# Kernel tuning notes

Hardware: AMD Instinct MI355X
Metric: run time of the kernel (lower is better)

The kernel has to match this reference:

```python
import jax, jax.numpy as jnp
import numpy as np

N_NODES = 50000
N_EDGES = 800000


def _glorot(key, shape):
    fan_in, fan_out = shape
    lim = float(np.sqrt(6.0 / (fan_in + fan_out)))
    return jax.random.uniform(key, shape, jnp.float32, -lim, lim)


def setup_inputs() -> dict:
    key = jax.random.key(0)
    ks = jax.random.split(key, 8)
    x = jax.random.normal(ks[0], (N_NODES, 2), jnp.float32)
    edge_index = jax.random.randint(ks[1], (2, N_EDGES), 0, N_NODES, jnp.int64)
    edge_weight = jax.random.uniform(ks[2], (N_EDGES,), jnp.float32)
    return {
        "x": x,
        "edge_index": edge_index,
        "edge_weight": edge_weight,
        "W1": _glorot(ks[3], (2, 128)),
        "b1": jnp.zeros((128,), jnp.float32),
        "W2": _glorot(ks[4], (128, 64)),
        "b2": jnp.zeros((64,), jnp.float32),
        "W3": _glorot(ks[5], (64, 1)),
        "b3": jnp.zeros((1,), jnp.float32),
    }


def _gcn_conv(x, W, b, src, dst, ew, n_nodes):
    # PyG GCNConv with normalize=False: out[i] = sum_{e:(j->i)} ew[e] * (x_j @ W) + b
    h = x @ W                       # [N, F_out] tiny GEMM
    msg = h[src] * ew[:, None]      # [E, F_out] gather + scale
    out = jax.ops.segment_sum(msg, dst, num_segments=n_nodes)  # scatter-add
    return out + b


def reference(x, edge_index, edge_weight, W1, b1, W2, b2, W3, b3):
    src, dst = edge_index[0], edge_index[1]  # source_to_target flow: aggregate at dst
    n = x.shape[0]
    h1 = jax.nn.relu(_gcn_conv(x, W1, b1, src, dst, edge_weight, n))
    # dropout is a no-op in eval mode
    h2 = jax.nn.relu(_gcn_conv(h1, W2, b2, src, dst, edge_weight, n))
    h3 = _gcn_conv(h2, W3, b3, src, dst, edge_weight, n)  # [N, 1]
    return h3.squeeze(-1)  # [N]
```

## Files before the change

### kernel.cpp

```cpp
#include <hip/hip_runtime.h>
#include <hip/hip_fp16.h>

#define N_NODES 50000
#define N_EDGES 800000
#define BSHIFT 8
#define NBKT ((N_NODES + 255) >> BSHIFT)
#define CAP 8192
#define P1_EDGES 4096
#define P1_BLOCKS ((N_EDGES + P1_EDGES - 1) / P1_EDGES)
#define BIN_THREADS 1024
#define SORT_THREADS 512
#define SORT_LDS_CAP 6144

__global__ void bin_edges(const int* __restrict__ src, const int* __restrict__ dst,
                          const float* __restrict__ ew, int* __restrict__ bcur,
                          unsigned* __restrict__ bpk, unsigned char* __restrict__ bdl) {
    __shared__ unsigned spk[P1_EDGES];
    __shared__ unsigned short sdst[P1_EDGES];
    __shared__ int cnt[NBKT];
    __shared__ int cbase[NBKT];
    int t = threadIdx.x;
    if (t < NBKT) cnt[t] = 0;
    __syncthreads();
    int e0 = blockIdx.x * P1_EDGES;
    for (int k = 0; k < P1_EDGES / BIN_THREADS; k++) {
        int i = k * BIN_THREADS + t;
        int e = e0 + i;
        if (e < N_EDGES) {
            int d = dst[e];
            unsigned hw = (unsigned)__half_as_ushort(__float2half(ew[e]));
            spk[i] = (unsigned)src[e] | (hw << 16);
            sdst[i] = (unsigned short)d;
            atomicAdd(&cnt[d >> BSHIFT], 1);
        }
    }
    __syncthreads();
    if (t < NBKT) {
        int v = cnt[t];
        int base = v ? atomicAdd(&bcur[t], v) : 0;
        cbase[t] = t * CAP + base;
        cnt[t] = 0;
    }
    __syncthreads();
    int nmax = N_EDGES - e0;
    if (nmax > P1_EDGES) nmax = P1_EDGES;
    for (int k = 0; k < P1_EDGES / BIN_THREADS; k++) {
        int i = k * BIN_THREADS + t;
        if (i < nmax) {
            int d = sdst[i];
            int b = d >> BSHIFT;
            int pos = cbase[b] + atomicAdd(&cnt[b], 1);
            bpk[pos] = spk[i];
            bdl[pos] = (unsigned char)(d & 255);
        }
    }
}

__global__ void sort_bucket(const int* __restrict__ bcur, const unsigned* __restrict__ bpk,
                            const unsigned char* __restrict__ bdl,
                            unsigned* __restrict__ sorted, int2* __restrict__ rowspan) {
    __shared__ unsigned spk[SORT_LDS_CAP];
    __shared__ unsigned char sdl[SORT_LDS_CAP];
    __shared__ int nh[256];
    __shared__ int scn[256];
    __shared__ int lcur[256];
    int b = blockIdx.x;
    int t = threadIdx.x;
    int base = b * CAP;
    int n = bcur[b];
    if (n > CAP) n = CAP;
    bool lds_path = (n <= SORT_LDS_CAP);
    if (t < 256) nh[t] = 0;
    __syncthreads();
    if (lds_path) {
        for (int e = t; e < n; e += SORT_THREADS) {
            spk[e] = bpk[base + e];
            unsigned char d = bdl[base + e];
            sdl[e] = d;
            atomicAdd(&nh[d], 1);
        }
    } else {
        for (int e = t; e < n; e += SORT_THREADS)
            atomicAdd(&nh[bdl[base + e]], 1);
    }
    __syncthreads();
    int v = 0;
    if (t < 256) { v = nh[t]; scn[t] = v; }
    __syncthreads();
    for (int off = 1; off < 256; off <<= 1) {
        int u = (t < 256 && t >= off) ? scn[t - off] : 0;
        __syncthreads();
        if (t < 256) scn[t] += u;
        __syncthreads();
    }
    if (t < 256) {
        int ex = scn[t] - v;
        int node = (b << BSHIFT) + t;
        if (node < N_NODES) rowspan[node] = make_int2(base + ex, base + ex + v);
        nh[t] = ex;
        lcur[t] = 0;
    }
    __syncthreads();
    if (lds_path) {
        for (int e = t; e < n; e += SORT_THREADS) {
            int dlow = sdl[e];
            int pos = base + nh[dlow] + atomicAdd(&lcur[dlow], 1);
            sorted[pos] = spk[e];
        }
    } else {
        for (int e = t; e < n; e += SORT_THREADS) {
            int dlow = bdl[base + e];
            int pos = base + nh[dlow] + atomicAdd(&lcur[dlow], 1);
            sorted[pos] = bpk[base + e];
        }
    }
}

__device__ __forceinline__ float edge_w(unsigned p) {
    return __half2float(__ushort_as_half((unsigned short)(p >> 16)));
}

#define L1_NODES_PER_BLOCK 32
__global__ void fused_l1(const int2* __restrict__ rowspan, const unsigned* __restrict__ sorted,
                         const float* __restrict__ x, const float* __restrict__ W1,
                         const float* __restrict__ b1, const float* __restrict__ W2,
                         __half* __restrict__ t2) {
    __shared__ float w2s[128 * 64];
    __shared__ float hls[4][8][128];
    for (int k = threadIdx.x; k < 128 * 64; k += 256) w2s[k] = W2[k];
    int wave = threadIdx.x >> 6;
    int lane = threadIdx.x & 63;
    float w1a = W1[lane],      w1b = W1[128 + lane];
    float w1c = W1[64 + lane], w1d = W1[192 + lane];
    float b1lo = b1[lane], b1hi = b1[64 + lane];
    __syncthreads();

    int sub = lane >> 4;
    int sl  = lane & 15;
    int base = blockIdx.x * L1_NODES_PER_BLOCK + wave * 8;

#pragma unroll
    for (int g = 0; g < 2; g++) {
        int gnode = base + g * 4 + sub;
        float a0 = 0.f, a1 = 0.f;
        if (gnode < N_NODES) {
            int2 sp = rowspan[gnode];
            for (int e = sp.x + sl; e < sp.y; e += 16) {
                unsigned p = sorted[e];
                float w = edge_w(p);
                float2 xv = ((const float2*)x)[p & 0xFFFF];
                a0 = fmaf(w, xv.x, a0);
                a1 = fmaf(w, xv.y, a1);
            }
        }
#pragma unroll
        for (int off = 1; off < 16; off <<= 1) {
            a0 += __shfl_xor(a0, off);
            a1 += __shfl_xor(a1, off);
        }
#pragma unroll
        for (int n = 0; n < 4; n++) {
            float an0 = __shfl(a0, 16 * n);
            float an1 = __shfl(a1, 16 * n);
            float hlo = fmaxf(fmaf(an0, w1a, fmaf(an1, w1b, b1lo)), 0.f);
            float hhi = fmaxf(fmaf(an0, w1c, fmaf(an1, w1d, b1hi)), 0.f);
            hls[wave][g * 4 + n][lane] = hlo;
            hls[wave][g * 4 + n][64 + lane] = hhi;
        }
    }
    float acc[8] = {0.f, 0.f, 0.f, 0.f, 0.f, 0.f, 0.f, 0.f};
#pragma unroll 2
    for (int k4 = 0; k4 < 32; k4++) {
        float w0 = w2s[(4 * k4 + 0) * 64 + lane];
        float w1 = w2s[(4 * k4 + 1) * 64 + lane];
        float w2 = w2s[(4 * k4 + 2) * 64 + lane];
        float w3 = w2s[(4 * k4 + 3) * 64 + lane];
#pragma unroll
        for (int n = 0; n < 8; n++) {
            float4 h = *(const float4*)&hls[wave][n][4 * k4];
            acc[n] = fmaf(h.x, w0, fmaf(h.y, w1, fmaf(h.z, w2, fmaf(h.w, w3, acc[n]))));
        }
    }
#pragma unroll
    for (int n = 0; n < 8; n++)
        if (base + n < N_NODES) t2[(base + n) * 64 + lane] = __float2half(acc[n]);
}

__global__ void gather2_dot3(const int2* __restrict__ rowspan, const unsigned* __restrict__ sorted,
                             const __half* __restrict__ t2, const float* __restrict__ b2,
                             const float* __restrict__ W3, float* __restrict__ t3) {
    int gtid = blockIdx.x * blockDim.x + threadIdx.x;
    int node = gtid >> 6;
    int lane = threadIdx.x & 63;
    if (node >= N_NODES) return;
    int eg  = lane >> 3;
    int fli = lane & 7;
    int2 sp = rowspan[node];
    float a0 = 0.f, a1 = 0.f, a2 = 0.f, a3 = 0.f, a4 = 0.f, a5 = 0.f, a6 = 0.f, a7 = 0.f;
    int e = sp.x + eg;
    for (; e + 8 < sp.y; e += 16) {
        unsigned p0 = sorted[e];
        unsigned p1 = sorted[e + 8];
        uint4 q0 = *(const uint4*)(t2 + (p0 & 0xFFFF) * 64 + fli * 8);
        uint4 q1 = *(const uint4*)(t2 + (p1 & 0xFFFF) * 64 + fli * 8);
        float w0 = edge_w(p0), w1 = edge_w(p1);
        float2 f;
        f = __half22float2(*(const __half2*)&q0.x); a0 = fmaf(w0, f.x, a0); a1 = fmaf(w0, f.y, a1);
        f = __half22float2(*(const __half2*)&q0.y); a2 = fmaf(w0, f.x, a2); a3 = fmaf(w0, f.y, a3);
        f = __half22float2(*(const __half2*)&q0.z); a4 = fmaf(w0, f.x, a4); a5 = fmaf(w0, f.y, a5);
        f = __half22float2(*(const __half2*)&q0.w); a6 = fmaf(w0, f.x, a6); a7 = fmaf(w0, f.y, a7);
        f = __half22float2(*(const __half2*)&q1.x); a0 = fmaf(w1, f.x, a0); a1 = fmaf(w1, f.y, a1);
        f = __half22float2(*(const __half2*)&q1.y); a2 = fmaf(w1, f.x, a2); a3 = fmaf(w1, f.y, a3);
        f = __half22float2(*(const __half2*)&q1.z); a4 = fmaf(w1, f.x, a4); a5 = fmaf(w1, f.y, a5);
        f = __half22float2(*(const __half2*)&q1.w); a6 = fmaf(w1, f.x, a6); a7 = fmaf(w1, f.y, a7);
    }
    if (e < sp.y) {
        unsigned p = sorted[e];
        uint4 q = *(const uint4*)(t2 + (p & 0xFFFF) * 64 + fli * 8);
        float w = edge_w(p);
        float2 f;
        f = __half22float2(*(const __half2*)&q.x); a0 = fmaf(w, f.x, a0); a1 = fmaf(w, f.y, a1);
        f = __half22float2(*(const __half2*)&q.y); a2 = fmaf(w, f.x, a2); a3 = fmaf(w, f.y, a3);
        f = __half22float2(*(const __half2*)&q.z); a4 = fmaf(w, f.x, a4); a5 = fmaf(w, f.y, a5);
        f = __half22float2(*(const __half2*)&q.w); a6 = fmaf(w, f.x, a6); a7 = fmaf(w, f.y, a7);
    }
#pragma unroll
    for (int off = 8; off < 64; off <<= 1) {
        a0 += __shfl_xor(a0, off); a1 += __shfl_xor(a1, off);
        a2 += __shfl_xor(a2, off); a3 += __shfl_xor(a3, off);
        a4 += __shfl_xor(a4, off); a5 += __shfl_xor(a5, off);
        a6 += __shfl_xor(a6, off); a7 += __shfl_xor(a7, off);
    }
    float4 bA = *(const float4*)(b2 + fli * 8);
    float4 bB = *(const float4*)(b2 + fli * 8 + 4);
    float4 wA = *(const float4*)(W3 + fli * 8);
    float4 wB = *(const float4*)(W3 + fli * 8 + 4);
    float h = fmaxf(a0 + bA.x, 0.f) * wA.x + fmaxf(a1 + bA.y, 0.f) * wA.y +
              fmaxf(a2 + bA.z, 0.f) * wA.z + fmaxf(a3 + bA.w, 0.f) * wA.w +
              fmaxf(a4 + bB.x, 0.f) * wB.x + fmaxf(a5 + bB.y, 0.f) * wB.y +
              fmaxf(a6 + bB.z, 0.f) * wB.z + fmaxf(a7 + bB.w, 0.f) * wB.w;
#pragma unroll
    for (int off = 1; off < 8; off <<= 1) h += __shfl_xor(h, off);
    if (lane == 0) t3[node] = h;
}

__global__ void gather3(const int2* __restrict__ rowspan, const unsigned* __restrict__ sorted,
                        const float* __restrict__ t3, const float* __restrict__ b3,
                        float* __restrict__ out) {
    int gtid = blockIdx.x * blockDim.x + threadIdx.x;
    int wid = gtid >> 6;
    int lane = threadIdx.x & 63;
    int sub = lane >> 4;
    int sl  = lane & 15;
    int node = wid * 4 + sub;
    if (node >= N_NODES) return;
    int2 sp = rowspan[node];
    float acc = 0.f;
    for (int e = sp.x + sl; e < sp.y; e += 16) {
        unsigned p = sorted[e];
        acc = fmaf(edge_w(p), t3[p & 0xFFFF], acc);
    }
#pragma unroll
    for (int off = 1; off < 16; off <<= 1) acc += __shfl_xor(acc, off);
    if (sl == 0) out[node] = acc + b3[0];
}

extern "C" void kernel_launch(void* const* d_in, const int* in_sizes, int n_in,
                              void* d_out, int out_size, void* d_ws, size_t ws_size,
                              hipStream_t stream) {
    const float* x  = (const float*)d_in[0];
    const int*   ei = (const int*)d_in[1];
    const float* ew = (const float*)d_in[2];
    const float* W1 = (const float*)d_in[3];
    const float* b1 = (const float*)d_in[4];
    const float* W2 = (const float*)d_in[5];
    const float* b2 = (const float*)d_in[6];
    const float* W3 = (const float*)d_in[7];
    const float* b3 = (const float*)d_in[8];
    float* out = (float*)d_out;

    const int* src = ei;
    const int* dst = ei + N_EDGES;

    char* p = (char*)d_ws;
    int*  bcur    = (int*)p;            p += NBKT * sizeof(int);
    p = (char*)(((uintptr_t)p + 15) & ~(uintptr_t)15);
    int2* rowspan = (int2*)p;           p += N_NODES * sizeof(int2);
    unsigned* bpk = (unsigned*)p;       p += (long)NBKT * CAP * sizeof(unsigned);
    unsigned char* bdl = (unsigned char*)p; p += (long)NBKT * CAP;
    p = (char*)(((uintptr_t)p + 15) & ~(uintptr_t)15);
    unsigned* sorted  = (unsigned*)p;   p += (long)NBKT * CAP * sizeof(unsigned);
    __half* t2    = (__half*)p;         p += 64L * N_NODES * sizeof(__half);
    float* t3     = (float*)p;          p += N_NODES * sizeof(float);

    hipMemsetAsync(bcur, 0, NBKT * sizeof(int), stream);

    bin_edges<<<P1_BLOCKS, BIN_THREADS, 0, stream>>>(src, dst, ew, bcur, bpk, bdl);
    sort_bucket<<<NBKT, SORT_THREADS, 0, stream>>>(bcur, bpk, bdl, sorted, rowspan);

    fused_l1<<<(N_NODES + L1_NODES_PER_BLOCK - 1) / L1_NODES_PER_BLOCK, 256, 0, stream>>>(
        rowspan, sorted, x, W1, b1, W2, t2);

    gather2_dot3<<<(N_NODES * 64 + 255) / 256, 256, 0, stream>>>(rowspan, sorted, t2, b2, W3, t3);

    gather3<<<((N_NODES + 3) / 4 * 64 + 255) / 256, 256, 0, stream>>>(rowspan, sorted, t3, b3, out);
}
```

Measured before the change: 160.4 us.

## Fuse bucket sort with layer-1 aggregation and W2 projection in one kernel

Merges the per-bucket counting sort with the first GCN layer. Each bucket block sorts its edges, then reuses the same LDS to load W2 and computes layer-1 aggregation plus the 128x64 projection for its 256 nodes. This removes one kernel launch and the rowspan reload, since the block keeps each node's span in LDS. In exchange, parallelism drops to about 196 blocks of 512 threads, each doing 8 serial passes, so GPU occupancy is low and the GEMM part may run serialized per bucket.

New measurement: 168.7 us. 1.05x slower.

```diff
diff --git a/kernel.cpp b/kernel.cpp
--- a/kernel.cpp
+++ b/kernel.cpp
@@ -9,7 +9,7 @@
 #define P1_EDGES 4096
 #define P1_BLOCKS ((N_EDGES + P1_EDGES - 1) / P1_EDGES)
 #define BIN_THREADS 1024
-#define SORT_THREADS 512
+#define SL_THREADS 512
 #define SORT_LDS_CAP 6144
 
 __global__ void bin_edges(const int* __restrict__ src, const int* __restrict__ dst,
@@ -56,31 +56,52 @@
     }
 }
 
-__global__ void sort_bucket(const int* __restrict__ bcur, const unsigned* __restrict__ bpk,
-                            const unsigned char* __restrict__ bdl,
-                            unsigned* __restrict__ sorted, int2* __restrict__ rowspan) {
-    __shared__ unsigned spk[SORT_LDS_CAP];
-    __shared__ unsigned char sdl[SORT_LDS_CAP];
-    __shared__ int nh[256];
-    __shared__ int scn[256];
-    __shared__ int lcur[256];
+__device__ __forceinline__ float edge_w(unsigned p) {
+    return __half2float(__ushort_as_half((unsigned short)(p >> 16)));
+}
+
+__global__ void sort_l1(const int* __restrict__ bcur, const unsigned* __restrict__ bpk,
+                        const unsigned char* __restrict__ bdl,
+                        unsigned* __restrict__ sorted, int2* __restrict__ rowspan,
+                        const float* __restrict__ x, const float* __restrict__ W1,
+                        const float* __restrict__ b1, const float* __restrict__ W2,
+                        __half* __restrict__ t2) {
+    __shared__ __align__(16) char smem[51200];
+    unsigned* spk = (unsigned*)smem;
+    float* w2s = (float*)smem;
+    unsigned char* sdl = (unsigned char*)(smem + 32768);
+    int* nh   = (int*)(smem + 32768 + 6144);
+    int* scn  = (int*)(smem + 32768 + 6144 + 1024);
+    int* lcur = (int*)(smem + 32768 + 6144 + 2048);
+    float* hls = (float*)(smem + 32768);
+    int* exs = (int*)(smem + 49152);
+    int* cns = (int*)(smem + 50176);
+
     int b = blockIdx.x;
     int t = threadIdx.x;
     int base = b * CAP;
+    int wave = t >> 6;
+    int lane = t & 63;
+
+    float w1a = W1[lane],      w1b = W1[128 + lane];
+    float w1c = W1[64 + lane], w1d = W1[192 + lane];
+    float b1lo = b1[lane], b1hi = b1[64 + lane];
+
     int n = bcur[b];
     if (n > CAP) n = CAP;
     bool lds_path = (n <= SORT_LDS_CAP);
     if (t < 256) nh[t] = 0;
     __syncthreads();
     if (lds_path) {
-        for (int e = t; e < n; e += SORT_THREADS) {
-            spk[e] = bpk[base + e];
+        for (int e = t; e < n; e += SL_THREADS) {
+            unsigned v = bpk[base + e];
+            spk[e] = v;
             unsigned char d = bdl[base + e];
             sdl[e] = d;
             atomicAdd(&nh[d], 1);
         }
     } else {
-        for (int e = t; e < n; e += SORT_THREADS)
+        for (int e = t; e < n; e += SL_THREADS)
             atomicAdd(&nh[bdl[base + e]], 1);
     }
     __syncthreads();
@@ -97,55 +118,41 @@
         int ex = scn[t] - v;
         int node = (b << BSHIFT) + t;
         if (node < N_NODES) rowspan[node] = make_int2(base + ex, base + ex + v);
+        exs[t] = ex;
+        cns[t] = v;
         nh[t] = ex;
         lcur[t] = 0;
     }
     __syncthreads();
     if (lds_path) {
-        for (int e = t; e < n; e += SORT_THREADS) {
+        for (int e = t; e < n; e += SL_THREADS) {
             int dlow = sdl[e];
             int pos = base + nh[dlow] + atomicAdd(&lcur[dlow], 1);
             sorted[pos] = spk[e];
         }
     } else {
-        for (int e = t; e < n; e += SORT_THREADS) {
+        for (int e = t; e < n; e += SL_THREADS) {
             int dlow = bdl[base + e];
             int pos = base + nh[dlow] + atomicAdd(&lcur[dlow], 1);
             sorted[pos] = bpk[base + e];
         }
     }
-}
-
-__device__ __forceinline__ float edge_w(unsigned p) {
-    return __half2float(__ushort_as_half((unsigned short)(p >> 16)));
-}
-
-#define L1_NODES_PER_BLOCK 32
-__global__ void fused_l1(const int2* __restrict__ rowspan, const unsigned* __restrict__ sorted,
-                         const float* __restrict__ x, const float* __restrict__ W1,
-                         const float* __restrict__ b1, const float* __restrict__ W2,
-                         __half* __restrict__ t2) {
-    __shared__ float w2s[128 * 64];
-    __shared__ float hls[4][8][128];
-    for (int k = threadIdx.x; k < 128 * 64; k += 256) w2s[k] = W2[k];
-    int wave = threadIdx.x >> 6;
-    int lane = threadIdx.x & 63;
-    float w1a = W1[lane],      w1b = W1[128 + lane];
-    float w1c = W1[64 + lane], w1d = W1[192 + lane];
-    float b1lo = b1[lane], b1hi = b1[64 + lane];
+    __syncthreads();
+    for (int k = t; k < 128 * 64; k += SL_THREADS) w2s[k] = W2[k];
     __syncthreads();
 
     int sub = lane >> 4;
     int sl  = lane & 15;
-    int base = blockIdx.x * L1_NODES_PER_BLOCK + wave * 8;
-
-#pragma unroll
-    for (int g = 0; g < 2; g++) {
-        int gnode = base + g * 4 + sub;
+    float* hw = hls + wave * 4 * 128;
+    for (int pass = 0; pass < 8; pass++) {
+        int nl_base = wave * 32 + pass * 4;
+        int gnl = nl_base + sub;
+        int gnode = (b << BSHIFT) + gnl;
         float a0 = 0.f, a1 = 0.f;
         if (gnode < N_NODES) {
-            int2 sp = rowspan[gnode];
-            for (int e = sp.x + sl; e < sp.y; e += 16) {
+            int beg = base + exs[gnl];
+            int end = beg + cns[gnl];
+            for (int e = beg + sl; e < end; e += 16) {
                 unsigned p = sorted[e];
                 float w = edge_w(p);
                 float2 xv = ((const float2*)x)[p & 0xFFFF];
@@ -159,31 +166,36 @@
             a1 += __shfl_xor(a1, off);
         }
 #pragma unroll
-        for (int n = 0; n < 4; n++) {
-            float an0 = __shfl(a0, 16 * n);
-            float an1 = __shfl(a1, 16 * n);
+        for (int nn = 0; nn < 4; nn++) {
+            float an0 = __shfl(a0, 16 * nn);
+            float an1 = __shfl(a1, 16 * nn);
             float hlo = fmaxf(fmaf(an0, w1a, fmaf(an1, w1b, b1lo)), 0.f);
             float hhi = fmaxf(fmaf(an0, w1c, fmaf(an1, w1d, b1hi)), 0.f);
-            hls[wave][g * 4 + n][lane] = hlo;
-            hls[wave][g * 4 + n][64 + lane] = hhi;
-        }
-    }
-    float acc[8] = {0.f, 0.f, 0.f, 0.f, 0.f, 0.f, 0.f, 0.f};
-#pragma unroll 2
-    for (int k4 = 0; k4 < 32; k4++) {
-        float w0 = w2s[(4 * k4 + 0) * 64 + lane];
-        float w1 = w2s[(4 * k4 + 1) * 64 + lane];
-        float w2 = w2s[(4 * k4 + 2) * 64 + lane];
-        float w3 = w2s[(4 * k4 + 3) * 64 + lane];
-#pragma unroll
-        for (int n = 0; n < 8; n++) {
-            float4 h = *(const float4*)&hls[wave][n][4 * k4];
-            acc[n] = fmaf(h.x, w0, fmaf(h.y, w1, fmaf(h.z, w2, fmaf(h.w, w3, acc[n]))));
-        }
-    }
-#pragma unroll
-    for (int n = 0; n < 8; n++)
-        if (base + n < N_NODES) t2[(base + n) * 64 + lane] = __float2half(acc[n]);
+            hw[nn * 128 + lane] = hlo;
+            hw[nn * 128 + 64 + lane] = hhi;
+        }
+        float acc0 = 0.f, acc1 = 0.f, acc2 = 0.f, acc3 = 0.f;
+#pragma unroll 4
+        for (int k4 = 0; k4 < 32; k4++) {
+            float w0 = w2s[(4 * k4 + 0) * 64 + lane];
+            float w1 = w2s[(4 * k4 + 1) * 64 + lane];
+            float w2 = w2s[(4 * k4 + 2) * 64 + lane];
+            float w3 = w2s[(4 * k4 + 3) * 64 + lane];
+            float4 h0 = *(const float4*)&hw[0 * 128 + 4 * k4];
+            float4 h1 = *(const float4*)&hw[1 * 128 + 4 * k4];
+            float4 h2 = *(const float4*)&hw[2 * 128 + 4 * k4];
+            float4 h3 = *(const float4*)&hw[3 * 128 + 4 * k4];
+            acc0 = fmaf(h0.x, w0, fmaf(h0.y, w1, fmaf(h0.z, w2, fmaf(h0.w, w3, acc0))));
+            acc1 = fmaf(h1.x, w0, fmaf(h1.y, w1, fmaf(h1.z, w2, fmaf(h1.w, w3, acc1))));
+            acc2 = fmaf(h2.x, w0, fmaf(h2.y, w1, fmaf(h2.z, w2, fmaf(h2.w, w3, acc2))));
+            acc3 = fmaf(h3.x, w0, fmaf(h3.y, w1, fmaf(h3.z, w2, fmaf(h3.w, w3, acc3))));
+        }
+        int gbase = (b << BSHIFT) + nl_base;
+        if (gbase + 0 < N_NODES) t2[(gbase + 0) * 64 + lane] = __float2half(acc0);
+        if (gbase + 1 < N_NODES) t2[(gbase + 1) * 64 + lane] = __float2half(acc1);
+        if (gbase + 2 < N_NODES) t2[(gbase + 2) * 64 + lane] = __float2half(acc2);
+        if (gbase + 3 < N_NODES) t2[(gbase + 3) * 64 + lane] = __float2half(acc3);
+    }
 }
 
 __global__ void gather2_dot3(const int2* __restrict__ rowspan, const unsigned* __restrict__ sorted,
@@ -296,10 +308,9 @@
     hipMemsetAsync(bcur, 0, NBKT * sizeof(int), stream);
 
     bin_edges<<<P1_BLOCKS, BIN_THREADS, 0, stream>>>(src, dst, ew, bcur, bpk, bdl);
-    sort_bucket<<<NBKT, SORT_THREADS, 0, stream>>>(bcur, bpk, bdl, sorted, rowspan);
-
-    fused_l1<<<(N_NODES + L1_NODES_PER_BLOCK - 1) / L1_NODES_PER_BLOCK, 256, 0, stream>>>(
-        rowspan, sorted, x, W1, b1, W2, t2);
+
+    sort_l1<<<NBKT, SL_THREADS, 0, stream>>>(bcur, bpk, bdl, sorted, rowspan,
+                                             x, W1, b1, W2, t2);
 
     gather2_dot3<<<(N_NODES * 64 + 255) / 256, 256, 0, stream>>>(rowspan, sorted, t2, b2, W3, t3);
 
```
